# Kernel optimization log

Measured on AMD Instinct MI355X. Metric: run time of the kernel, lower is better.

## Reference

```python
import jax, jax.numpy as jnp
import numpy as np

NUM_HEADS = 16
NEG = -1e9


def setup_inputs() -> dict:
    key = jax.random.key(0)
    ks = jax.random.split(key, 9)
    B, S, D = 1, 4096, 1024
    s = 1.0 / np.sqrt(D)
    return {
        "x": jax.random.normal(ks[0], (B, S, D), dtype=jnp.float32),
        "wq": jax.random.normal(ks[1], (D, D), dtype=jnp.float32) * s,
        "bq": jax.random.normal(ks[2], (D,), dtype=jnp.float32) * s,
        "wk": jax.random.normal(ks[3], (D, D), dtype=jnp.float32) * s,
        "bk": jax.random.normal(ks[4], (D,), dtype=jnp.float32) * s,
        "wv": jax.random.normal(ks[5], (D, D), dtype=jnp.float32) * s,
        "bv": jax.random.normal(ks[6], (D,), dtype=jnp.float32) * s,
        "wo": jax.random.normal(ks[7], (D, D), dtype=jnp.float32) * s,
        "bo": jax.random.normal(ks[8], (D,), dtype=jnp.float32) * s,
    }


def reference(x, wq, bq, wk, bk, wv, bv, wo, bo):
    B, S, D = x.shape
    H = NUM_HEADS
    hs = D // H
    # torch Linear: y = x @ W^T + b
    q = x @ wq.T + bq
    k = x @ wk.T + bk
    v = x @ wv.T + bv
    # [B, S, D] -> [B, H, S, hs]
    q = q.reshape(B, S, H, hs).transpose(0, 2, 1, 3)
    k = k.reshape(B, S, H, hs).transpose(0, 2, 1, 3)
    v = v.reshape(B, S, H, hs).transpose(0, 2, 1, 3)
    scores = jnp.einsum("bhqd,bhkd->bhqk", q, k) / jnp.sqrt(jnp.asarray(hs, x.dtype))
    causal = jnp.tril(jnp.ones((S, S), dtype=bool))  # True = keep
    scores = jnp.where(causal, scores, jnp.asarray(NEG, x.dtype))
    weights = jax.nn.softmax(scores, axis=-1)
    out = jnp.einsum("bhqk,bhkd->bhqd", weights, v)
    out = out.transpose(0, 2, 1, 3).reshape(B, S, D)
    return out @ wo.T + bo
```

## Files before the change

kernel.cpp:

```cpp
#include <hip/hip_runtime.h>

#define SEQ 4096
#define DM  1024
#define NH  16
#define HS  64
#define LDQK 2048

typedef __attribute__((ext_vector_type(8))) _Float16 f16x8;
typedef __attribute__((ext_vector_type(4))) _Float16 f16x4;
typedef __attribute__((ext_vector_type(4))) float    f32x4;

#define MFMA16(a, b, c) __builtin_amdgcn_mfma_f32_16x16x32_f16((a), (b), (c), 0, 0, 0)

#define AS1(p) ((const __attribute__((address_space(1))) void*)(p))
#define AS3(p) ((__attribute__((address_space(3))) void*)(p))

#define DPP_ROR_F(x, N) __int_as_float(__builtin_amdgcn_update_dpp( \
    0, __float_as_int(x), 0x120 + (N), 0xF, 0xF, false))

__device__ __forceinline__ float red16_add(float x) {
    x += DPP_ROR_F(x, 1);
    x += DPP_ROR_F(x, 2);
    x += DPP_ROR_F(x, 4);
    x += DPP_ROR_F(x, 8);
    return x;
}

__global__ __launch_bounds__(256) void cast_all(
    const float* __restrict__ x,
    const float* __restrict__ wq, const float* __restrict__ wk,
    const float* __restrict__ wv, const float* __restrict__ wo,
    _Float16* __restrict__ xb, _Float16* __restrict__ wqkb,
    _Float16* __restrict__ wvb, _Float16* __restrict__ wob)
{
    const float* s; _Float16* d; int i;
    if (blockIdx.y == 0) {
        s = x; d = xb;
        i = blockIdx.x * 1024 + threadIdx.x * 4;
    } else {
        int wsel = blockIdx.x >> 10;
        int bx   = blockIdx.x & 1023;
        switch (wsel) {
            case 0:  s = wq; d = wqkb;               break;
            case 1:  s = wk; d = wqkb + (1u << 20);  break;
            case 2:  s = wv; d = wvb;                break;
            default: s = wo; d = wob;                break;
        }
        i = bx * 1024 + threadIdx.x * 4;
    }
    float4 v = *reinterpret_cast<const float4*>(s + i);
    f16x4 o = {(_Float16)v.x, (_Float16)v.y, (_Float16)v.z, (_Float16)v.w};
    *reinterpret_cast<f16x4*>(d + i) = o;
}

template <int BM, int BIAS_ROW, typename OUT_T>
__global__ __launch_bounds__(256, 2) void gemm_lds(
    const _Float16* __restrict__ A,
    const _Float16* __restrict__ W,
    const float*    __restrict__ bias_lo,
    const float*    __restrict__ bias_hi,
    OUT_T* __restrict__ C,
    int M, int N, int K,
    float scale_lo, float scale_hi, int nsplit)
{
    constexpr int MI = BM / 32;
    __shared__ _Float16 As[BM][64];
    __shared__ _Float16 Bs[128][64];

    const int t    = threadIdx.x;
    const int w    = t >> 6;
    const int lane = t & 63;
    const int q    = lane >> 4;
    const int l    = lane & 15;
    const int m0   = blockIdx.y * BM;
    const int n0   = blockIdx.x * 128;
    const int wm   = (w & 1) * (BM / 2);
    const int wn   = (w >> 1) * 64;

    const float* bias  = (n0 < nsplit) ? bias_lo : bias_hi;
    const int    nbase = (n0 < nsplit) ? 0 : nsplit;
    const float  scale = (n0 < nsplit) ? scale_lo : scale_hi;

    const int srow = lane >> 3;
    const int scol = (lane & 7) * 8;

    f32x4 acc[MI][4];
    #pragma unroll
    for (int i = 0; i < MI; ++i)
        #pragma unroll
        for (int j = 0; j < 4; ++j) acc[i][j] = (f32x4){0.f, 0.f, 0.f, 0.f};

    for (int k0 = 0; k0 < K; k0 += 64) {
        __syncthreads();
        #pragma unroll
        for (int j = 0; j < BM / 32; ++j) {
            int c = w * (BM / 32) + j;
            __builtin_amdgcn_global_load_lds(
                AS1(A + (size_t)(m0 + c * 8 + srow) * K + k0 + scol),
                AS3((char*)&As[0][0] + c * 1024), 16, 0, 0);
        }
        #pragma unroll
        for (int j = 0; j < 4; ++j) {
            int c = w * 4 + j;
            __builtin_amdgcn_global_load_lds(
                AS1(W + (size_t)(n0 + c * 8 + srow) * K + k0 + scol),
                AS3((char*)&Bs[0][0] + c * 1024), 16, 0, 0);
        }
        __syncthreads();

        #pragma unroll
        for (int ks = 0; ks < 64; ks += 32) {
            f16x8 af[MI], bf[4];
            #pragma unroll
            for (int i = 0; i < MI; ++i)
                af[i] = *reinterpret_cast<const f16x8*>(&As[wm + i * 16 + l][ks + q * 8]);
            #pragma unroll
            for (int j = 0; j < 4; ++j)
                bf[j] = *reinterpret_cast<const f16x8*>(&Bs[wn + j * 16 + l][ks + q * 8]);
            #pragma unroll
            for (int i = 0; i < MI; ++i)
                #pragma unroll
                for (int j = 0; j < 4; ++j)
                    acc[i][j] = MFMA16(af[i], bf[j], acc[i][j]);
        }
    }

    #pragma unroll
    for (int i = 0; i < MI; ++i) {
        #pragma unroll
        for (int j = 0; j < 4; ++j) {
            int gnb = n0 + wn + j * 16 + l;
            float bc2 = BIAS_ROW ? 0.f : bias[gnb - nbase];
            #pragma unroll
            for (int r = 0; r < 4; ++r) {
                int gm = m0 + wm + i * 16 + q * 4 + r;
                float bb = BIAS_ROW ? bias[gm] : bc2;
                C[(size_t)gm * N + gnb] = (OUT_T)((acc[i][j][r] + bb) * scale);
            }
        }
    }
}

#define APAD 72

__global__ __launch_bounds__(256, 4) void attn_mfma(
    const _Float16* __restrict__ Qg,
    const _Float16* __restrict__ Kg,
    const _Float16* __restrict__ Vt,
    _Float16* __restrict__ O)
{
    __shared__ _Float16 Qs[64][APAD];
    __shared__ _Float16 Ks[4][16][APAD];
    __shared__ _Float16 Vs[64][APAD];
    __shared__ _Float16 Ps[64][APAD];

    const int t    = threadIdx.x;
    const int h    = blockIdx.x;
    const int by   = blockIdx.y;
    const int qb   = (by < 32) ? by : 95 - by;
    const int w    = t >> 6;
    const int lane = t & 63;
    const int q    = lane >> 4;
    const int l    = lane & 15;
    const int sr   = t >> 3;
    const int sc   = (t & 7) * 8;
    const int kj   = sr & 3;
    const int kn   = sr >> 2;

    *reinterpret_cast<uint4*>(&Qs[sr][sc]) =
        *reinterpret_cast<const uint4*>(Qg + (size_t)(qb * 64 + sr) * LDQK + h * 64 + sc);
    *reinterpret_cast<uint4*>(&Qs[sr + 32][sc]) =
        *reinterpret_cast<const uint4*>(Qg + (size_t)(qb * 64 + sr + 32) * LDQK + h * 64 + sc);

    uint4 kr0 = *reinterpret_cast<const uint4*>(Kg + (size_t)(sr) * LDQK + h * 64 + sc);
    uint4 kr1 = *reinterpret_cast<const uint4*>(Kg + (size_t)(sr + 32) * LDQK + h * 64 + sc);
    uint4 vr0 = *reinterpret_cast<const uint4*>(Vt + (size_t)(h * 64 + sr) * SEQ + sc);
    uint4 vr1 = *reinterpret_cast<const uint4*>(Vt + (size_t)(h * 64 + sr + 32) * SEQ + sc);

    float l_acc[4] = {0.f, 0.f, 0.f, 0.f};
    f32x4 oacc[4];
    #pragma unroll
    for (int nt = 0; nt < 4; ++nt) oacc[nt] = (f32x4){0.f, 0.f, 0.f, 0.f};

    __syncthreads();
    f16x8 aq0 = *reinterpret_cast<const f16x8*>(&Qs[w * 16 + l][q * 8]);
    f16x8 aq1 = *reinterpret_cast<const f16x8*>(&Qs[w * 16 + l][32 + q * 8]);

    const int qrow_base = qb * 64 + w * 16 + q * 4;

    for (int kt = 0; kt <= qb; ++kt) {
        __syncthreads();
        *reinterpret_cast<uint4*>(&Ks[kj][kn][sc])     = kr0;
        *reinterpret_cast<uint4*>(&Ks[kj][kn + 8][sc]) = kr1;
        *reinterpret_cast<uint4*>(&Vs[sr][sc])         = vr0;
        *reinterpret_cast<uint4*>(&Vs[sr + 32][sc])    = vr1;
        if (kt < qb) {
            kr0 = *reinterpret_cast<const uint4*>(
                Kg + (size_t)((kt + 1) * 64 + sr) * LDQK + h * 64 + sc);
            kr1 = *reinterpret_cast<const uint4*>(
                Kg + (size_t)((kt + 1) * 64 + sr + 32) * LDQK + h * 64 + sc);
            vr0 = *reinterpret_cast<const uint4*>(
                Vt + (size_t)(h * 64 + sr) * SEQ + (kt + 1) * 64 + sc);
            vr1 = *reinterpret_cast<const uint4*>(
                Vt + (size_t)(h * 64 + sr + 32) * SEQ + (kt + 1) * 64 + sc);
        }
        __syncthreads();

        f32x4 s[4];
        __builtin_amdgcn_s_setprio(1);
        #pragma unroll
        for (int jt = 0; jt < 4; ++jt) {
            f16x8 bk0 = *reinterpret_cast<const f16x8*>(&Ks[jt][l][q * 8]);
            f16x8 bk1 = *reinterpret_cast<const f16x8*>(&Ks[jt][l][32 + q * 8]);
            f32x4 z = (f32x4){0.f, 0.f, 0.f, 0.f};
            z = MFMA16(aq0, bk0, z);
            z = MFMA16(aq1, bk1, z);
            s[jt] = z;
        }
        __builtin_amdgcn_s_setprio(0);

        const bool diag = (kt == qb);

        #pragma unroll
        for (int r = 0; r < 4; ++r) {
            float p0 = s[0][r], p1 = s[1][r], p2 = s[2][r], p3 = s[3][r];
            if (diag) {
                const int qg = qrow_base + r;
                const int kg = kt * 64 + 4 * l;
                p0 = (kg + 0 <= qg) ? p0 : -1e30f;
                p1 = (kg + 1 <= qg) ? p1 : -1e30f;
                p2 = (kg + 2 <= qg) ? p2 : -1e30f;
                p3 = (kg + 3 <= qg) ? p3 : -1e30f;
            }
            p0 = __builtin_amdgcn_exp2f(p0 - 4.f);
            p1 = __builtin_amdgcn_exp2f(p1 - 4.f);
            p2 = __builtin_amdgcn_exp2f(p2 - 4.f);
            p3 = __builtin_amdgcn_exp2f(p3 - 4.f);
            l_acc[r] += (p0 + p1) + (p2 + p3);
            f16x4 pk = {(_Float16)p0, (_Float16)p1, (_Float16)p2, (_Float16)p3};
            *reinterpret_cast<f16x4*>(&Ps[w * 16 + q * 4 + r][4 * l]) = pk;
        }

        f16x8 ap0 = *reinterpret_cast<const f16x8*>(&Ps[w * 16 + l][q * 8]);
        f16x8 ap1 = *reinterpret_cast<const f16x8*>(&Ps[w * 16 + l][32 + q * 8]);
        __builtin_amdgcn_s_setprio(1);
        #pragma unroll
        for (int nt = 0; nt < 4; ++nt) {
            f16x8 bv0 = *reinterpret_cast<const f16x8*>(&Vs[nt * 16 + l][q * 8]);
            f16x8 bv1 = *reinterpret_cast<const f16x8*>(&Vs[nt * 16 + l][32 + q * 8]);
            oacc[nt] = MFMA16(ap0, bv0, oacc[nt]);
            oacc[nt] = MFMA16(ap1, bv1, oacc[nt]);
        }
        __builtin_amdgcn_s_setprio(0);
    }

    #pragma unroll
    for (int r = 0; r < 4; ++r) {
        float inv = 1.f / red16_add(l_acc[r]);
        size_t row = (size_t)(qb * 64 + w * 16 + q * 4 + r) * DM + h * 64;
        #pragma unroll
        for (int nt = 0; nt < 4; ++nt)
            O[row + nt * 16 + l] = (_Float16)(oacc[nt][r] * inv);
    }
}

extern "C" void kernel_launch(void* const* d_in, const int* in_sizes, int n_in,
                              void* d_out, int out_size, void* d_ws, size_t ws_size,
                              hipStream_t stream)
{
    const float* x  = (const float*)d_in[0];
    const float* wq = (const float*)d_in[1];
    const float* bq = (const float*)d_in[2];
    const float* wk = (const float*)d_in[3];
    const float* bk = (const float*)d_in[4];
    const float* wv = (const float*)d_in[5];
    const float* bv = (const float*)d_in[6];
    const float* wo = (const float*)d_in[7];
    const float* bo = (const float*)d_in[8];
    float* out = (float*)d_out;

    char* ws = (char*)d_ws;
    _Float16* xb   = (_Float16*)(ws);
    _Float16* wqkb = (_Float16*)(ws + (8ull  << 20));
    _Float16* wvb  = (_Float16*)(ws + (12ull << 20));
    _Float16* wob  = (_Float16*)(ws + (14ull << 20));
    _Float16* QKb  = (_Float16*)(ws + (16ull << 20));
    _Float16* Vtb  = (_Float16*)(ws + (32ull << 20));
    _Float16* Ab   = (_Float16*)(ws + (40ull << 20));

    cast_all<<<dim3(SEQ * DM / 1024, 2), dim3(256), 0, stream>>>(
        x, wq, wk, wv, wo, xb, wqkb, wvb, wob);

    gemm_lds<128, 0, _Float16><<<dim3(2048 / 128, SEQ / 128), dim3(256), 0, stream>>>(
        xb, wqkb, bq, bk, QKb, SEQ, 2048, DM,
        0.18033688011112042f, 1.0f, 1024);

    gemm_lds<64, 1, _Float16><<<dim3(SEQ / 128, DM / 64), dim3(256), 0, stream>>>(
        wvb, xb, bv, bv, Vtb, DM, SEQ, DM, 1.0f, 1.0f, 1 << 30);

    attn_mfma<<<dim3(NH, 64), dim3(256), 0, stream>>>(QKb, QKb + 1024, Vtb, Ab);

    gemm_lds<64, 0, float><<<dim3(DM / 128, SEQ / 64), dim3(256), 0, stream>>>(
        Ab, wob, bo, bo, out, SEQ, DM, DM, 1.0f, 1.0f, 1 << 30);
}
```

Baseline: 216.3 us.

## Double-buffer GEMM LDS tiles and XOR-swizzle columns to avoid bank conflicts

The projection GEMM now keeps two LDS buffers for the A and W tiles. It issues the global-to-LDS loads for the next k-slice right after the barrier, so they can overlap with the MFMA work on the current slice, and it needs only one barrier per iteration. It also XOR-swizzles the 16-byte column chunks by row when staging and reading, to cut LDS bank conflicts on the fragment loads. This doubles the GEMM's LDS footprint, which may limit occupancy. The overlap also depends on the compiler not placing a full vmcnt wait before the LDS reads.

```diff
diff --git a/kernel.cpp b/kernel.cpp
--- a/kernel.cpp
+++ b/kernel.cpp
@@ -64,8 +64,8 @@
     float scale_lo, float scale_hi, int nsplit)
 {
     constexpr int MI = BM / 32;
-    __shared__ _Float16 As[BM][64];
-    __shared__ _Float16 Bs[128][64];
+    __shared__ _Float16 As[2][BM][64];
+    __shared__ _Float16 Bs[2][128][64];
 
     const int t    = threadIdx.x;
     const int w    = t >> 6;
@@ -82,47 +82,61 @@
     const float  scale = (n0 < nsplit) ? scale_lo : scale_hi;
 
     const int srow = lane >> 3;
-    const int scol = (lane & 7) * 8;
-
-    f32x4 acc[MI][4];
-    #pragma unroll
-    for (int i = 0; i < MI; ++i)
-        #pragma unroll
-        for (int j = 0; j < 4; ++j) acc[i][j] = (f32x4){0.f, 0.f, 0.f, 0.f};
-
-    for (int k0 = 0; k0 < K; k0 += 64) {
-        __syncthreads();
+    const int scol = ((lane & 7) ^ (lane >> 3)) * 8;
+
+    auto stage = [&](int p, int k0) {
         #pragma unroll
         for (int j = 0; j < BM / 32; ++j) {
             int c = w * (BM / 32) + j;
             __builtin_amdgcn_global_load_lds(
                 AS1(A + (size_t)(m0 + c * 8 + srow) * K + k0 + scol),
-                AS3((char*)&As[0][0] + c * 1024), 16, 0, 0);
+                AS3((char*)&As[p][0][0] + c * 1024), 16, 0, 0);
         }
         #pragma unroll
         for (int j = 0; j < 4; ++j) {
             int c = w * 4 + j;
             __builtin_amdgcn_global_load_lds(
                 AS1(W + (size_t)(n0 + c * 8 + srow) * K + k0 + scol),
-                AS3((char*)&Bs[0][0] + c * 1024), 16, 0, 0);
-        }
+                AS3((char*)&Bs[p][0][0] + c * 1024), 16, 0, 0);
+        }
+    };
+
+    f32x4 acc[MI][4];
+    #pragma unroll
+    for (int i = 0; i < MI; ++i)
+        #pragma unroll
+        for (int j = 0; j < 4; ++j) acc[i][j] = (f32x4){0.f, 0.f, 0.f, 0.f};
+
+    stage(0, 0);
+    int p = 0;
+    for (int k0 = 0; k0 < K; k0 += 64) {
         __syncthreads();
+        if (k0 + 64 < K) stage(p ^ 1, k0 + 64);
 
         #pragma unroll
         for (int ks = 0; ks < 64; ks += 32) {
             f16x8 af[MI], bf[4];
             #pragma unroll
-            for (int i = 0; i < MI; ++i)
-                af[i] = *reinterpret_cast<const f16x8*>(&As[wm + i * 16 + l][ks + q * 8]);
+            for (int i = 0; i < MI; ++i) {
+                int r = wm + i * 16 + l;
+                af[i] = *reinterpret_cast<const f16x8*>(
+                    (const char*)&As[p][0][0] + r * 128 +
+                    ((((ks >> 3) + q) ^ (l & 7)) << 4));
+            }
             #pragma unroll
-            for (int j = 0; j < 4; ++j)
-                bf[j] = *reinterpret_cast<const f16x8*>(&Bs[wn + j * 16 + l][ks + q * 8]);
+            for (int j = 0; j < 4; ++j) {
+                int r = wn + j * 16 + l;
+                bf[j] = *reinterpret_cast<const f16x8*>(
+                    (const char*)&Bs[p][0][0] + r * 128 +
+                    ((((ks >> 3) + q) ^ (l & 7)) << 4));
+            }
             #pragma unroll
             for (int i = 0; i < MI; ++i)
                 #pragma unroll
                 for (int j = 0; j < 4; ++j)
                     acc[i][j] = MFMA16(af[i], bf[j], acc[i][j]);
         }
+        p ^= 1;
     }
 
     #pragma unroll
```

New measurement: 205.7 us. 1.05x faster.
